# Optimization experiments

Measured on AMD Instinct MI355X. Metric: run time of the kernel, lower is better.

Reference implementation:

```python
import jax, jax.numpy as jnp
import numpy as np

N_EMBD = 1024
HEAD_SIZE = 64


def setup_inputs() -> dict:
    key = jax.random.key(0)
    k1, k2, k3, k4 = jax.random.split(key, 4)
    x = jax.random.normal(k1, (8, 2048, N_EMBD), dtype=jnp.float32)
    # torch Linear(n_embd, head_size, bias=False): y = x @ W.T with W [out,in].
    # Store as [in, out] so y = x @ W. Scale init like torch default (~1/sqrt(in)).
    s = 1.0 / np.sqrt(N_EMBD)
    Wk = jax.random.uniform(k2, (N_EMBD, HEAD_SIZE), jnp.float32, -s, s)
    Wq = jax.random.uniform(k3, (N_EMBD, HEAD_SIZE), jnp.float32, -s, s)
    Wv = jax.random.uniform(k4, (N_EMBD, HEAD_SIZE), jnp.float32, -s, s)
    return {"x": x, "Wk": Wk, "Wq": Wq, "Wv": Wv}


def reference(x, Wk, Wq, Wv):
    # x: [B,T,C]
    B, T, C = x.shape
    k = x @ Wk  # [B,T,H]
    q = x @ Wq  # [B,T,H]
    v = x @ Wv  # [B,T,H]
    scale = HEAD_SIZE ** -0.5
    wei = jnp.einsum('bth,bsh->bts', q, k) * scale  # [B,T,T]
    causal = jnp.tril(jnp.ones((T, T), dtype=bool))  # [T,T]
    wei = jnp.where(causal[None, :, :], wei, -jnp.inf)
    wei = jax.nn.softmax(wei, axis=-1)
    # dropout(p=0.2) is identity in eval mode (deterministic baseline)
    out = jnp.einsum('bts,bsh->bth', wei, v)  # [B,T,H]
    return out
```

## Files before the change

kernel.cpp:

```cpp
#include <hip/hip_runtime.h>
#include <hip/hip_bf16.h>

#define B_DIM 8
#define T_DIM 2048
#define C_DIM 1024
#define H_DIM 64
#define BT (B_DIM * T_DIM)

typedef __attribute__((ext_vector_type(8))) short bf16x8;
typedef __attribute__((ext_vector_type(4))) float f32x4;

__device__ __forceinline__ ushort f2bf(float f) {
    __hip_bfloat16 h = __float2bfloat16(f);
    return *reinterpret_cast<ushort*>(&h);
}
__device__ __forceinline__ unsigned int packbf(float a, float b) {
    return (unsigned int)f2bf(a) | ((unsigned int)f2bf(b) << 16);
}

__global__ __launch_bounds__(256) void wt_convert_kernel(
    const float* __restrict__ Wk, const float* __restrict__ Wq,
    const float* __restrict__ Wv, ushort* __restrict__ wt)
{
    const int n = blockIdx.x;
    const float* src = (n < 64) ? Wk : (n < 128) ? Wq : Wv;
    const float scale = (n >= 64 && n < 128) ? 0.125f * 1.4426950408889634f : 1.0f;
    const int col = n & 63;
    for (int k = threadIdx.x; k < C_DIM; k += 256)
        wt[(size_t)n * C_DIM + k] = f2bf(src[(size_t)k * H_DIM + col] * scale);
}

__global__ __launch_bounds__(512, 4) void qkv_gemm_kernel(
    const float* __restrict__ x, const ushort* __restrict__ wt,
    ushort* __restrict__ kb, ushort* __restrict__ qb, ushort* __restrict__ vt)
{
    __shared__ ushort Xf[2][2][4 * 64 * 8];
    __shared__ float  Ls[256 * 25];
    const int tid = threadIdx.x;
    const int wave = tid >> 6, lane = tid & 63;
    const int kh = wave >> 2, nh = wave & 3;
    const int col = lane & 15, quad = lane >> 4;
    const int r0 = blockIdx.x * 32;
    const int kbase = kh * 512;

    f32x4 acc[2][3];
    #pragma unroll
    for (int m = 0; m < 2; ++m)
        #pragma unroll
        for (int j = 0; j < 3; ++j) acc[m][j] = (f32x4){0.f, 0.f, 0.f, 0.f};

    const float* xsrc = x + (size_t)(r0 + (nh >> 1) * 16 + col) * C_DIM
                          + kbase + (nh & 1) * 32 + quad * 8;
    ushort* xdst[2] = {&Xf[0][kh][(nh * 64 + lane) * 8],
                       &Xf[1][kh][(nh * 64 + lane) * 8]};

    const ushort* wsrc[3][2];
    #pragma unroll
    for (int j = 0; j < 3; ++j)
        #pragma unroll
        for (int ks = 0; ks < 2; ++ks)
            wsrc[j][ks] = wt + (size_t)((nh * 3 + j) * 16 + col) * C_DIM
                             + kbase + ks * 32 + quad * 8;

    {
        const float4 f0 = *(const float4*)(xsrc);
        const float4 f1 = *(const float4*)(xsrc + 4);
        uint4 u;
        u.x = packbf(f0.x, f0.y); u.y = packbf(f0.z, f0.w);
        u.z = packbf(f1.x, f1.y); u.w = packbf(f1.z, f1.w);
        *(uint4*)xdst[0] = u;
    }
    bf16x8 wcur[3][2];
    #pragma unroll
    for (int j = 0; j < 3; ++j)
        #pragma unroll
        for (int ks = 0; ks < 2; ++ks)
            wcur[j][ks] = *(const bf16x8*)(wsrc[j][ks]);
    __syncthreads();

    for (int i = 0; i < 8; ++i) {
        const int b = i & 1;
        bf16x8 wnxt[3][2];
        float4 nf0, nf1;
        if (i < 7) {
            const int k1 = (i + 1) * 64;
            #pragma unroll
            for (int j = 0; j < 3; ++j)
                #pragma unroll
                for (int ks = 0; ks < 2; ++ks)
                    wnxt[j][ks] = *(const bf16x8*)(wsrc[j][ks] + k1);
            nf0 = *(const float4*)(xsrc + k1);
            nf1 = *(const float4*)(xsrc + k1 + 4);
        }
        bf16x8 a[2][2];
        #pragma unroll
        for (int mf = 0; mf < 2; ++mf)
            #pragma unroll
            for (int ks = 0; ks < 2; ++ks)
                a[mf][ks] = *(const bf16x8*)&Xf[b][kh][((mf * 2 + ks) * 64 + lane) * 8];
        #pragma unroll
        for (int ks = 0; ks < 2; ++ks)
            #pragma unroll
            for (int j = 0; j < 3; ++j) {
                acc[0][j] = __builtin_amdgcn_mfma_f32_16x16x32_bf16(a[0][ks], wcur[j][ks], acc[0][j], 0, 0, 0);
                acc[1][j] = __builtin_amdgcn_mfma_f32_16x16x32_bf16(a[1][ks], wcur[j][ks], acc[1][j], 0, 0, 0);
            }
        if (i < 7) {
            #pragma unroll
            for (int j = 0; j < 3; ++j)
                #pragma unroll
                for (int ks = 0; ks < 2; ++ks)
                    wcur[j][ks] = wnxt[j][ks];
            uint4 u;
            u.x = packbf(nf0.x, nf0.y); u.y = packbf(nf0.z, nf0.w);
            u.z = packbf(nf1.x, nf1.y); u.w = packbf(nf1.z, nf1.w);
            *(uint4*)xdst[b ^ 1] = u;
        }
        __syncthreads();
    }

    if (kh == 1) {
        float* dst = &Ls[(tid & 255) * 25];
        #pragma unroll
        for (int mf = 0; mf < 2; ++mf)
            #pragma unroll
            for (int j = 0; j < 3; ++j)
                #pragma unroll
                for (int r = 0; r < 4; ++r)
                    dst[(mf * 3 + j) * 4 + r] = acc[mf][j][r];
    }
    __syncthreads();
    if (kh == 0) {
        const float* srcl = &Ls[tid * 25];
        #pragma unroll
        for (int mf = 0; mf < 2; ++mf)
            #pragma unroll
            for (int j = 0; j < 3; ++j)
                #pragma unroll
                for (int r = 0; r < 4; ++r)
                    acc[mf][j][r] += srcl[(mf * 3 + j) * 4 + r];

        #pragma unroll
        for (int j = 0; j < 3; ++j) {
            const int nt = nh * 3 + j;
            #pragma unroll
            for (int mf = 0; mf < 2; ++mf) {
                const int rbase = r0 + mf * 16 + quad * 4;
                if (nt < 4) {
                    const int n = nt * 16 + col;
                    #pragma unroll
                    for (int r = 0; r < 4; ++r)
                        kb[(size_t)(rbase + r) * H_DIM + n] = f2bf(acc[mf][j][r]);
                } else if (nt < 8) {
                    const int n = nt * 16 + col - 64;
                    #pragma unroll
                    for (int r = 0; r < 4; ++r)
                        qb[(size_t)(rbase + r) * H_DIM + n] = f2bf(acc[mf][j][r]);
                } else {
                    const int h = nt * 16 + col - 128;
                    const int vbatch = rbase >> 11, vrow = rbase & (T_DIM - 1);
                    ushort u4[4] = {f2bf(acc[mf][j][0]), f2bf(acc[mf][j][1]),
                                    f2bf(acc[mf][j][2]), f2bf(acc[mf][j][3])};
                    unsigned long long uu; __builtin_memcpy(&uu, u4, 8);
                    *(unsigned long long*)(vt + ((size_t)vbatch * H_DIM + h) * T_DIM + vrow) = uu;
                }
            }
        }
    }
}

__global__ __launch_bounds__(256, 4) void attn_kernel(
    const ushort* __restrict__ kb, const ushort* __restrict__ qb,
    const ushort* __restrict__ vt, float* __restrict__ out)
{
    __shared__ unsigned int Ps[8][16 * 34];
    __shared__ float Om[4][64][17];
    __shared__ float Mm[4][16], Lm[4][16];

    const int tid = threadIdx.x;
    const int wave = tid >> 6, lane = tid & 63;
    const int col = lane & 15, quad = lane >> 4;
    const int batch = blockIdx.x & 7;
    const int qtile = 127 - (blockIdx.x >> 3);
    const int q0 = qtile * 16;

    const ushort* kbase = kb + (size_t)batch * T_DIM * H_DIM;
    const ushort* vbase = vt + (size_t)batch * H_DIM * T_DIM;

    const size_t qoff = (size_t)(batch * T_DIM + q0 + col) * H_DIM + quad * 8;
    const bf16x8 bq0 = *(const bf16x8*)(qb + qoff);
    const bf16x8 bq1 = *(const bf16x8*)(qb + qoff + 32);

    float mA = -INFINITY, lA = 0.f, mB = -INFINITY, lB = 0.f;
    f32x4 oA[4], oB[4];
    #pragma unroll
    for (int i = 0; i < 4; ++i) {
        oA[i] = (f32x4){0.f, 0.f, 0.f, 0.f};
        oB[i] = (f32x4){0.f, 0.f, 0.f, 0.f};
    }

    const int ntiles = (q0 + 16 + 63) >> 6;

    auto qk_tile = [&](int kb0, f32x4* s) {
        #pragma unroll
        for (int mt = 0; mt < 4; ++mt) s[mt] = (f32x4){0.f, 0.f, 0.f, 0.f};
        #pragma unroll
        for (int ks = 0; ks < 2; ++ks) {
            const bf16x8 bq = ks ? bq1 : bq0;
            #pragma unroll
            for (int mt = 0; mt < 4; ++mt) {
                const bf16x8 ak = *(const bf16x8*)
                    (kbase + (size_t)(kb0 + mt * 16 + col) * H_DIM + ks * 32 + quad * 8);
                s[mt] = __builtin_amdgcn_mfma_f32_16x16x32_bf16(ak, bq, s[mt], 0, 0, 0);
            }
        }
        if (kb0 + 63 > q0) {
            const int kq = kb0 + quad * 4 - q0 - col;
            #pragma unroll
            for (int mt = 0; mt < 4; ++mt)
                #pragma unroll
                for (int reg = 0; reg < 4; ++reg)
                    if (kq + mt * 16 + reg > 0) s[mt][reg] = -INFINITY;
        }
    };

    auto sm_pv = [&](int kb0, f32x4* s, float& m_, float& l_, f32x4* o_,
                     unsigned int* psw) {
        float mr = -INFINITY;
        #pragma unroll
        for (int mt = 0; mt < 4; ++mt)
            #pragma unroll
            for (int reg = 0; reg < 4; ++reg) mr = fmaxf(mr, s[mt][reg]);
        mr = fmaxf(mr, __shfl_xor(mr, 16));
        mr = fmaxf(mr, __shfl_xor(mr, 32));
        const float mn = fmaxf(m_, mr);
        const float corr = exp2f(m_ - mn);
        float sum = 0.f;
        #pragma unroll
        for (int mt = 0; mt < 4; ++mt)
            #pragma unroll
            for (int reg = 0; reg < 4; ++reg) {
                const float pv = exp2f(s[mt][reg] - mn);
                s[mt][reg] = pv;
                sum += pv;
            }
        sum += __shfl_xor(sum, 16);
        sum += __shfl_xor(sum, 32);
        l_ = l_ * corr + sum;
        m_ = mn;
        #pragma unroll
        for (int ht = 0; ht < 4; ++ht) o_[ht] *= corr;
        #pragma unroll
        for (int mt = 0; mt < 4; ++mt) {
            uint2 w2;
            w2.x = packbf(s[mt][0], s[mt][1]);
            w2.y = packbf(s[mt][2], s[mt][3]);
            *(uint2*)&psw[col * 34 + mt * 8 + quad * 2] = w2;
        }
        #pragma unroll
        for (int ks2 = 0; ks2 < 2; ++ks2) {
            const uint2 ra = *(const uint2*)&psw[col * 34 + ks2 * 16 + quad * 4];
            const uint2 rb = *(const uint2*)&psw[col * 34 + ks2 * 16 + quad * 4 + 2];
            unsigned int ub[4] = {ra.x, ra.y, rb.x, rb.y};
            bf16x8 bp; __builtin_memcpy(&bp, ub, 16);
            #pragma unroll
            for (int ht = 0; ht < 4; ++ht) {
                const bf16x8 av = *(const bf16x8*)
                    (vbase + (size_t)(ht * 16 + col) * T_DIM + kb0 + ks2 * 32 + quad * 8);
                o_[ht] = __builtin_amdgcn_mfma_f32_16x16x32_bf16(av, bp, o_[ht], 0, 0, 0);
            }
        }
    };

    for (int t = wave; t < ntiles; t += 8) {
        const int t2 = t + 4;
        const bool hasB = t2 < ntiles;
        f32x4 sA[4], sB[4];
        qk_tile(t * 64, sA);
        if (hasB) qk_tile(t2 * 64, sB);
        sm_pv(t * 64, sA, mA, lA, oA, &Ps[wave][0]);
        if (hasB) sm_pv(t2 * 64, sB, mB, lB, oB, &Ps[wave + 4][0]);
    }

    const float M = fmaxf(mA, mB);
    const float eA = (mA == -INFINITY) ? 0.f : exp2f(mA - M);
    const float eB = (mB == -INFINITY) ? 0.f : exp2f(mB - M);
    const float L = lA * eA + lB * eB;
    #pragma unroll
    for (int ht = 0; ht < 4; ++ht)
        #pragma unroll
        for (int reg = 0; reg < 4; ++reg)
            Om[wave][ht * 16 + quad * 4 + reg][col] = oA[ht][reg] * eA + oB[ht][reg] * eB;
    if (lane < 16) { Mm[wave][lane] = M; Lm[wave][lane] = L; }
    __syncthreads();
    {
        const int q = tid >> 4, hb = tid & 15;
        const float Mb = fmaxf(fmaxf(Mm[0][q], Mm[1][q]), fmaxf(Mm[2][q], Mm[3][q]));
        const float a0 = exp2f(Mm[0][q] - Mb), a1 = exp2f(Mm[1][q] - Mb);
        const float a2 = exp2f(Mm[2][q] - Mb), a3 = exp2f(Mm[3][q] - Mb);
        const float Lb = Lm[0][q] * a0 + Lm[1][q] * a1 + Lm[2][q] * a2 + Lm[3][q] * a3;
        const float rL = 1.0f / Lb;
        float* orow = out + (size_t)(batch * T_DIM + q0 + q) * H_DIM;
        #pragma unroll
        for (int i = 0; i < 4; ++i) {
            const int h = hb + 16 * i;
            orow[h] = (Om[0][h][q] * a0 + Om[1][h][q] * a1 +
                       Om[2][h][q] * a2 + Om[3][h][q] * a3) * rL;
        }
    }
}

extern "C" void kernel_launch(void* const* d_in, const int* in_sizes, int n_in,
                              void* d_out, int out_size, void* d_ws, size_t ws_size,
                              hipStream_t stream)
{
    const float* x  = (const float*)d_in[0];
    const float* Wk = (const float*)d_in[1];
    const float* Wq = (const float*)d_in[2];
    const float* Wv = (const float*)d_in[3];

    ushort* kbuf = (ushort*)d_ws;
    ushort* qbuf = kbuf + (size_t)BT * H_DIM;
    ushort* vtb  = qbuf + (size_t)BT * H_DIM;
    ushort* wt   = vtb  + (size_t)BT * H_DIM;

    wt_convert_kernel<<<192, 256, 0, stream>>>(Wk, Wq, Wv, wt);
    qkv_gemm_kernel<<<BT / 32, 512, 0, stream>>>(x, wt, kbuf, qbuf, vtb);
    attn_kernel<<<B_DIM * 128, 256, 0, stream>>>(kbuf, qbuf, vtb, (float*)d_out);
}
```

Baseline: 162.9 us.

## Compute softmax row sums via MFMA with ones row in padded V

```diff
diff --git a/kernel.cpp b/kernel.cpp
--- a/kernel.cpp
+++ b/kernel.cpp
@@ -6,6 +6,7 @@
 #define C_DIM 1024
 #define H_DIM 64
 #define BT (B_DIM * T_DIM)
+#define VT_ROWS 80
 
 typedef __attribute__((ext_vector_type(8))) short bf16x8;
 typedef __attribute__((ext_vector_type(4))) float f32x4;
@@ -20,14 +21,24 @@
 
 __global__ __launch_bounds__(256) void wt_convert_kernel(
     const float* __restrict__ Wk, const float* __restrict__ Wq,
-    const float* __restrict__ Wv, ushort* __restrict__ wt)
+    const float* __restrict__ Wv, ushort* __restrict__ wt,
+    ushort* __restrict__ vt)
 {
-    const int n = blockIdx.x;
-    const float* src = (n < 64) ? Wk : (n < 128) ? Wq : Wv;
-    const float scale = (n >= 64 && n < 128) ? 0.125f * 1.4426950408889634f : 1.0f;
-    const int col = n & 63;
-    for (int k = threadIdx.x; k < C_DIM; k += 256)
-        wt[(size_t)n * C_DIM + k] = f2bf(src[(size_t)k * H_DIM + col] * scale);
+    const int b = blockIdx.x;
+    if (b < 192) {
+        const int n = b;
+        const float* src = (n < 64) ? Wk : (n < 128) ? Wq : Wv;
+        const float scale = (n >= 64 && n < 128) ? 0.125f * 1.4426950408889634f : 1.0f;
+        const int col = n & 63;
+        for (int k = threadIdx.x; k < C_DIM; k += 256)
+            wt[(size_t)n * C_DIM + k] = f2bf(src[(size_t)k * H_DIM + col] * scale);
+    } else {
+        const int j = b - 192;
+        const int batch = j >> 4, row = 64 + (j & 15);
+        const ushort val = (row == 64) ? (ushort)0x3F80 : (ushort)0;
+        ushort* dst = vt + ((size_t)batch * VT_ROWS + row) * T_DIM;
+        for (int k = threadIdx.x; k < T_DIM; k += 256) dst[k] = val;
+    }
 }
 
 __global__ __launch_bounds__(512, 4) void qkv_gemm_kernel(
@@ -162,7 +173,7 @@
                     ushort u4[4] = {f2bf(acc[mf][j][0]), f2bf(acc[mf][j][1]),
                                     f2bf(acc[mf][j][2]), f2bf(acc[mf][j][3])};
                     unsigned long long uu; __builtin_memcpy(&uu, u4, 8);
-                    *(unsigned long long*)(vt + ((size_t)vbatch * H_DIM + h) * T_DIM + vrow) = uu;
+                    *(unsigned long long*)(vt + ((size_t)vbatch * VT_ROWS + h) * T_DIM + vrow) = uu;
                 }
             }
         }
@@ -173,7 +184,7 @@
     const ushort* __restrict__ kb, const ushort* __restrict__ qb,
     const ushort* __restrict__ vt, float* __restrict__ out)
 {
-    __shared__ unsigned int Ps[8][16 * 34];
+    __shared__ unsigned int Ps[4][16 * 34];
     __shared__ float Om[4][64][17];
     __shared__ float Mm[4][16], Lm[4][16];
 
@@ -185,23 +196,23 @@
     const int q0 = qtile * 16;
 
     const ushort* kbase = kb + (size_t)batch * T_DIM * H_DIM;
-    const ushort* vbase = vt + (size_t)batch * H_DIM * T_DIM;
+    const ushort* vbase = vt + (size_t)batch * VT_ROWS * T_DIM;
 
     const size_t qoff = (size_t)(batch * T_DIM + q0 + col) * H_DIM + quad * 8;
     const bf16x8 bq0 = *(const bf16x8*)(qb + qoff);
     const bf16x8 bq1 = *(const bf16x8*)(qb + qoff + 32);
 
-    float mA = -INFINITY, lA = 0.f, mB = -INFINITY, lB = 0.f;
-    f32x4 oA[4], oB[4];
-    #pragma unroll
-    for (int i = 0; i < 4; ++i) {
-        oA[i] = (f32x4){0.f, 0.f, 0.f, 0.f};
-        oB[i] = (f32x4){0.f, 0.f, 0.f, 0.f};
-    }
+    float m_ = -INFINITY;
+    f32x4 o_[4], lacc = (f32x4){0.f, 0.f, 0.f, 0.f};
+    #pragma unroll
+    for (int i = 0; i < 4; ++i) o_[i] = (f32x4){0.f, 0.f, 0.f, 0.f};
 
     const int ntiles = (q0 + 16 + 63) >> 6;
-
-    auto qk_tile = [&](int kb0, f32x4* s) {
+    unsigned int* psw = &Ps[wave][0];
+
+    for (int t = wave; t < ntiles; t += 4) {
+        const int kb0 = t * 64;
+        f32x4 s[4];
         #pragma unroll
         for (int mt = 0; mt < 4; ++mt) s[mt] = (f32x4){0.f, 0.f, 0.f, 0.f};
         #pragma unroll
@@ -214,6 +225,13 @@
                 s[mt] = __builtin_amdgcn_mfma_f32_16x16x32_bf16(ak, bq, s[mt], 0, 0, 0);
             }
         }
+        bf16x8 av[5][2];
+        #pragma unroll
+        for (int ht = 0; ht < 5; ++ht)
+            #pragma unroll
+            for (int ks2 = 0; ks2 < 2; ++ks2)
+                av[ht][ks2] = *(const bf16x8*)
+                    (vbase + (size_t)(ht * 16 + col) * T_DIM + kb0 + ks2 * 32 + quad * 8);
         if (kb0 + 63 > q0) {
             const int kq = kb0 + quad * 4 - q0 - col;
             #pragma unroll
@@ -222,10 +240,6 @@
                 for (int reg = 0; reg < 4; ++reg)
                     if (kq + mt * 16 + reg > 0) s[mt][reg] = -INFINITY;
         }
-    };
-
-    auto sm_pv = [&](int kb0, f32x4* s, float& m_, float& l_, f32x4* o_,
-                     unsigned int* psw) {
         float mr = -INFINITY;
         #pragma unroll
         for (int mt = 0; mt < 4; ++mt)
@@ -235,21 +249,15 @@
         mr = fmaxf(mr, __shfl_xor(mr, 32));
         const float mn = fmaxf(m_, mr);
         const float corr = exp2f(m_ - mn);
-        float sum = 0.f;
+        m_ = mn;
         #pragma unroll
         for (int mt = 0; mt < 4; ++mt)
             #pragma unroll
-            for (int reg = 0; reg < 4; ++reg) {
-                const float pv = exp2f(s[mt][reg] - mn);
-                s[mt][reg] = pv;
-                sum += pv;
-            }
-        sum += __shfl_xor(sum, 16);
-        sum += __shfl_xor(sum, 32);
-        l_ = l_ * corr + sum;
-        m_ = mn;
+            for (int reg = 0; reg < 4; ++reg)
+                s[mt][reg] = exp2f(s[mt][reg] - mn);
         #pragma unroll
         for (int ht = 0; ht < 4; ++ht) o_[ht] *= corr;
+        lacc *= corr;
         #pragma unroll
         for (int mt = 0; mt < 4; ++mt) {
             uint2 w2;
@@ -264,34 +272,18 @@
             unsigned int ub[4] = {ra.x, ra.y, rb.x, rb.y};
             bf16x8 bp; __builtin_memcpy(&bp, ub, 16);
             #pragma unroll
-            for (int ht = 0; ht < 4; ++ht) {
-                const bf16x8 av = *(const bf16x8*)
-                    (vbase + (size_t)(ht * 16 + col) * T_DIM + kb0 + ks2 * 32 + quad * 8);
-                o_[ht] = __builtin_amdgcn_mfma_f32_16x16x32_bf16(av, bp, o_[ht], 0, 0, 0);
-            }
-        }
-    };
-
-    for (int t = wave; t < ntiles; t += 8) {
-        const int t2 = t + 4;
-        const bool hasB = t2 < ntiles;
-        f32x4 sA[4], sB[4];
-        qk_tile(t * 64, sA);
-        if (hasB) qk_tile(t2 * 64, sB);
-        sm_pv(t * 64, sA, mA, lA, oA, &Ps[wave][0]);
-        if (hasB) sm_pv(t2 * 64, sB, mB, lB, oB, &Ps[wave + 4][0]);
-    }
-
-    const float M = fmaxf(mA, mB);
-    const float eA = (mA == -INFINITY) ? 0.f : exp2f(mA - M);
-    const float eB = (mB == -INFINITY) ? 0.f : exp2f(mB - M);
-    const float L = lA * eA + lB * eB;
+            for (int ht = 0; ht < 4; ++ht)
+                o_[ht] = __builtin_amdgcn_mfma_f32_16x16x32_bf16(av[ht][ks2], bp, o_[ht], 0, 0, 0);
+            lacc = __builtin_amdgcn_mfma_f32_16x16x32_bf16(av[4][ks2], bp, lacc, 0, 0, 0);
+        }
+    }
+
     #pragma unroll
     for (int ht = 0; ht < 4; ++ht)
         #pragma unroll
         for (int reg = 0; reg < 4; ++reg)
-            Om[wave][ht * 16 + quad * 4 + reg][col] = oA[ht][reg] * eA + oB[ht][reg] * eB;
-    if (lane < 16) { Mm[wave][lane] = M; Lm[wave][lane] = L; }
+            Om[wave][ht * 16 + quad * 4 + reg][col] = o_[ht][reg];
+    if (quad == 0) { Mm[wave][col] = m_; Lm[wave][col] = lacc[0]; }
     __syncthreads();
     {
         const int q = tid >> 4, hb = tid & 15;
@@ -322,9 +314,9 @@
     ushort* kbuf = (ushort*)d_ws;
     ushort* qbuf = kbuf + (size_t)BT * H_DIM;
     ushort* vtb  = qbuf + (size_t)BT * H_DIM;
-    ushort* wt   = vtb  + (size_t)BT * H_DIM;
-
-    wt_convert_kernel<<<192, 256, 0, stream>>>(Wk, Wq, Wv, wt);
+    ushort* wt   = vtb  + (size_t)B_DIM * VT_ROWS * T_DIM;
+
+    wt_convert_kernel<<<320, 256, 0, stream>>>(Wk, Wq, Wv, wt, vtb);
     qkv_gemm_kernel<<<BT / 32, 512, 0, stream>>>(x, wt, kbuf, qbuf, vtb);
     attn_kernel<<<B_DIM * 128, 256, 0, stream>>>(kbuf, qbuf, vtb, (float*)d_out);
 }
```

Result: no change. 165.7 us (+1.7%).
